# Kernel tuning notes

Measured on AMD Instinct MI355X. Metric: run time of the kernel, lower is better.

The kernel has to match this reference:

```python
import jax, jax.numpy as jnp
import numpy as np

G = 128          # number of point-cloud groups
DOWNSAMPLE = 256 # points per group
D = 256          # feature dim


def _pairwise_dist(x, y):
    # x: [G, n, d], y: [G, m, d] -> Euclidean distances [G, n, m]
    x2 = jnp.sum(x * x, axis=-1)[:, :, None]
    y2 = jnp.sum(y * y, axis=-1)[:, None, :]
    d2 = jnp.maximum(x2 + y2 - 2.0 * jnp.einsum('gnd,gmd->gnm', x, y), 0.0)
    # safe sqrt (zero diagonal has zero distance, avoid NaN grads)
    return jnp.where(d2 > 0, jnp.sqrt(jnp.where(d2 > 0, d2, 1.0)), 0.0)


def setup_inputs() -> dict:
    key = jax.random.key(0)
    k1, k2 = jax.random.split(key)
    inp = jax.random.normal(k1, (G * DOWNSAMPLE, D), dtype=jnp.float32)
    tgt = jax.random.normal(k2, (G * DOWNSAMPLE, D), dtype=jnp.float32)
    return {"input": inp, "target": tgt, "downsample": DOWNSAMPLE}


def reference(input, target, downsample):
    # MMDLoss.forward: reshape to (-1, downsample, D), batched energy distance, mean
    x = input.reshape(-1, downsample, input.shape[-1])   # [G, n, D]
    y = target.reshape(-1, downsample, target.shape[-1]) # [G, m, D]
    # Energy distance (geomloss 'energy' kernel k(x,y) = -||x-y||, uniform weights):
    # L = mean_ij ||x_i - y_j|| - 0.5 mean_ij ||x_i - x_j|| - 0.5 mean_ij ||y_i - y_j||
    d_xy = jnp.mean(_pairwise_dist(x, y), axis=(1, 2))  # [G]
    d_xx = jnp.mean(_pairwise_dist(x, x), axis=(1, 2))  # [G]
    d_yy = jnp.mean(_pairwise_dist(y, y), axis=(1, 2))  # [G]
    loss_per_group = d_xy - 0.5 * d_xx - 0.5 * d_yy
    return jnp.mean(loss_per_group)
```

## Files before the change

kernel.cpp:

```cpp
#include <hip/hip_runtime.h>
#include <hip/hip_bf16.h>
#include <stdint.h>
#include <string.h>

typedef __attribute__((ext_vector_type(8))) short short8;
typedef __attribute__((ext_vector_type(4))) float floatx4;

#define NPTS 256
#define DIM  256
#define TILE 128
#define BK   32
#define NIT  (DIM / BK)

static __device__ __forceinline__ uint32_t cvt2(float a, float b) {
    __hip_bfloat162 h = __float22bfloat162_rn(float2{a, b});
    uint32_t d;
    memcpy(&d, &h, 4);
    return d;
}
static __device__ __forceinline__ float sq8(const float4 u, const float4 v) {
    return u.x * u.x + u.y * u.y + u.z * u.z + u.w * u.w +
           v.x * v.x + v.y * v.y + v.z * v.z + v.w * v.w;
}

__global__ __launch_bounds__(512, 4)
void mmd_pipe(const float* __restrict__ X, const float* __restrict__ Y,
              float* __restrict__ out, float scale, int G) {
    int g, t;
    const int f = blockIdx.x;
    if ((G & 7) == 0) { const int xcd = f & 7, j = f >> 3; g = (j / 10) * 8 + xcd; t = j % 10; }
    else              { g = f / 10; t = f % 10; }

    int ptype, ti, tj; float w;
    if (t < 4)      { ptype = 0; ti = t >> 1; tj = t & 1; w = 1.0f; }
    else if (t < 7) { int u = t - 4; ptype = 1; ti = (u == 2); tj = (u >= 1); w = (u == 1) ? -1.0f : -0.5f; }
    else            { int u = t - 7; ptype = 2; ti = (u == 2); tj = (u >= 1); w = (u == 1) ? -1.0f : -0.5f; }

    const float *Pf, *Qf;
    if (ptype == 0)      { Pf = X; Qf = Y; }
    else if (ptype == 1) { Pf = X; Qf = X; }
    else                 { Pf = Y; Qf = Y; }
    const bool symdiag = (ptype != 0) && (ti == tj);

    const size_t prow0 = (size_t)g * NPTS + (size_t)ti * TILE;
    const size_t qrow0 = (size_t)g * NPTS + (size_t)tj * TILE;

    __shared__ __align__(16) uint16_t As[2][TILE * BK];
    __shared__ __align__(16) uint16_t Bs[2][TILE * BK];
    __shared__ float rnorm[TILE];
    __shared__ float cnorm[TILE];
    __shared__ float wpart[8];

    const int tid  = threadIdx.x;
    const int lane = tid & 63;
    const int wv   = tid >> 6;
    const int quad = lane >> 4;
    const int l15  = lane & 15;
    const int rowbase = (wv & 3) * 32;
    const int colbase = (wv >> 2) * 64;
    const int rsw = (quad ^ ((l15 >> 1) & 3)) * 8;

    const int prow = tid >> 2;
    const int pchk = tid & 3;
    const float* gA = Pf + (prow0 + prow) * DIM + pchk * 8;
    const int woff = prow * BK + ((pchk ^ ((prow >> 1) & 3)) * 8);

    floatx4 acc[2][4];
    #pragma unroll
    for (int i = 0; i < 2; ++i)
        #pragma unroll
        for (int j = 0; j < 4; ++j) acc[i][j] = (floatx4)0.0f;

    float sqp = 0.0f;

    if (symdiag) {
        float4 ra0 = *(const float4*)(gA);
        float4 ra1 = *(const float4*)(gA + 4);
        {
            uint4 pa;
            sqp += sq8(ra0, ra1);
            pa.x = cvt2(ra0.x, ra0.y); pa.y = cvt2(ra0.z, ra0.w);
            pa.z = cvt2(ra1.x, ra1.y); pa.w = cvt2(ra1.z, ra1.w);
            *(uint4*)&As[0][woff] = pa;
        }
        ra0 = *(const float4*)(gA + BK);
        ra1 = *(const float4*)(gA + BK + 4);

        #pragma unroll
        for (int it = 0; it < NIT; ++it) {
            const int b = it & 1;
            __syncthreads();

            short8 af[2], bfr[4];
            #pragma unroll
            for (int mi = 0; mi < 2; ++mi)
                af[mi] = *(const short8*)&As[b][(rowbase + mi * 16 + l15) * BK + rsw];
            #pragma unroll
            for (int ni = 0; ni < 4; ++ni)
                bfr[ni] = *(const short8*)&As[b][(colbase + ni * 16 + l15) * BK + rsw];

            if (it < NIT - 1) {
                uint4 pa;
                sqp += sq8(ra0, ra1);
                pa.x = cvt2(ra0.x, ra0.y); pa.y = cvt2(ra0.z, ra0.w);
                pa.z = cvt2(ra1.x, ra1.y); pa.w = cvt2(ra1.z, ra1.w);
                *(uint4*)&As[b ^ 1][woff] = pa;
            }
            if (it < NIT - 2) {
                const int k0 = (it + 2) * BK;
                ra0 = *(const float4*)(gA + k0);
                ra1 = *(const float4*)(gA + k0 + 4);
            }

            #pragma unroll
            for (int mi = 0; mi < 2; ++mi)
                #pragma unroll
                for (int ni = 0; ni < 4; ++ni)
                    acc[mi][ni] = __builtin_amdgcn_mfma_f32_16x16x32_bf16(
                        af[mi], bfr[ni], acc[mi][ni], 0, 0, 0);
        }

        sqp += __shfl_xor(sqp, 1); sqp += __shfl_xor(sqp, 2);
        if ((tid & 3) == 0) rnorm[prow] = sqp;
        __syncthreads();

        float lsum = 0.0f;
        #pragma unroll
        for (int mi = 0; mi < 2; ++mi) {
            #pragma unroll
            for (int i = 0; i < 4; ++i) {
                const int r = rowbase + mi * 16 + quad * 4 + i;
                const float rv = rnorm[r];
                #pragma unroll
                for (int ni = 0; ni < 4; ++ni) {
                    const int c = colbase + ni * 16 + l15;
                    float d2 = rv + rnorm[c] - 2.0f * acc[mi][ni][i];
                    float s = sqrtf(fmaxf(d2, 0.0f));
                    if (r == c) s = 0.0f;
                    lsum += s;
                }
            }
        }
        #pragma unroll
        for (int off = 32; off; off >>= 1) lsum += __shfl_down(lsum, off);
        if (lane == 0) wpart[wv] = lsum;
        __syncthreads();
        if (tid == 0) {
            float bs = 0.0f;
            #pragma unroll
            for (int i = 0; i < 8; ++i) bs += wpart[i];
            atomicAdd(out, bs * (w * scale));
        }
        return;
    }

    const float* gB = Qf + (qrow0 + prow) * DIM + pchk * 8;
    float sqq = 0.0f;

    float4 ra0 = *(const float4*)(gA);
    float4 ra1 = *(const float4*)(gA + 4);
    float4 rb0 = *(const float4*)(gB);
    float4 rb1 = *(const float4*)(gB + 4);
    {
        uint4 pa, pb;
        sqp += sq8(ra0, ra1);
        sqq += sq8(rb0, rb1);
        pa.x = cvt2(ra0.x, ra0.y); pa.y = cvt2(ra0.z, ra0.w);
        pa.z = cvt2(ra1.x, ra1.y); pa.w = cvt2(ra1.z, ra1.w);
        pb.x = cvt2(rb0.x, rb0.y); pb.y = cvt2(rb0.z, rb0.w);
        pb.z = cvt2(rb1.x, rb1.y); pb.w = cvt2(rb1.z, rb1.w);
        *(uint4*)&As[0][woff] = pa;
        *(uint4*)&Bs[0][woff] = pb;
    }
    ra0 = *(const float4*)(gA + BK);
    ra1 = *(const float4*)(gA + BK + 4);
    rb0 = *(const float4*)(gB + BK);
    rb1 = *(const float4*)(gB + BK + 4);

    #pragma unroll
    for (int it = 0; it < NIT; ++it) {
        const int b = it & 1;
        __syncthreads();

        short8 af[2], bfr[4];
        #pragma unroll
        for (int mi = 0; mi < 2; ++mi)
            af[mi] = *(const short8*)&As[b][(rowbase + mi * 16 + l15) * BK + rsw];
        #pragma unroll
        for (int ni = 0; ni < 4; ++ni)
            bfr[ni] = *(const short8*)&Bs[b][(colbase + ni * 16 + l15) * BK + rsw];

        if (it < NIT - 1) {
            uint4 pa, pb;
            sqp += sq8(ra0, ra1);
            sqq += sq8(rb0, rb1);
            pa.x = cvt2(ra0.x, ra0.y); pa.y = cvt2(ra0.z, ra0.w);
            pa.z = cvt2(ra1.x, ra1.y); pa.w = cvt2(ra1.z, ra1.w);
            pb.x = cvt2(rb0.x, rb0.y); pb.y = cvt2(rb0.z, rb0.w);
            pb.z = cvt2(rb1.x, rb1.y); pb.w = cvt2(rb1.z, rb1.w);
            *(uint4*)&As[b ^ 1][woff] = pa;
            *(uint4*)&Bs[b ^ 1][woff] = pb;
        }
        if (it < NIT - 2) {
            const int k0 = (it + 2) * BK;
            ra0 = *(const float4*)(gA + k0);
            ra1 = *(const float4*)(gA + k0 + 4);
            rb0 = *(const float4*)(gB + k0);
            rb1 = *(const float4*)(gB + k0 + 4);
        }

        #pragma unroll
        for (int mi = 0; mi < 2; ++mi)
            #pragma unroll
            for (int ni = 0; ni < 4; ++ni)
                acc[mi][ni] = __builtin_amdgcn_mfma_f32_16x16x32_bf16(
                    af[mi], bfr[ni], acc[mi][ni], 0, 0, 0);
    }

    sqp += __shfl_xor(sqp, 1); sqp += __shfl_xor(sqp, 2);
    sqq += __shfl_xor(sqq, 1); sqq += __shfl_xor(sqq, 2);
    if ((tid & 3) == 0) { rnorm[prow] = sqp; cnorm[prow] = sqq; }
    __syncthreads();

    float lsum = 0.0f;
    #pragma unroll
    for (int mi = 0; mi < 2; ++mi) {
        #pragma unroll
        for (int i = 0; i < 4; ++i) {
            const int r = rowbase + mi * 16 + quad * 4 + i;
            const float rv = rnorm[r];
            #pragma unroll
            for (int ni = 0; ni < 4; ++ni) {
                const int c = colbase + ni * 16 + l15;
                float d2 = rv + cnorm[c] - 2.0f * acc[mi][ni][i];
                float s = sqrtf(fmaxf(d2, 0.0f));
                lsum += s;
            }
        }
    }
    #pragma unroll
    for (int off = 32; off; off >>= 1) lsum += __shfl_down(lsum, off);
    if (lane == 0) wpart[wv] = lsum;
    __syncthreads();
    if (tid == 0) {
        float bs = 0.0f;
        #pragma unroll
        for (int i = 0; i < 8; ++i) bs += wpart[i];
        atomicAdd(out, bs * (w * scale));
    }
}

extern "C" void kernel_launch(void* const* d_in, const int* in_sizes, int n_in,
                              void* d_out, int out_size, void* d_ws, size_t ws_size,
                              hipStream_t stream) {
    const float* X = (const float*)d_in[0];
    const float* Y = (const float*)d_in[1];
    const int total_elems = in_sizes[0];
    const int G = total_elems / (NPTS * DIM);

    float* out = (float*)d_out;
    hipMemsetAsync(out, 0, sizeof(float) * out_size, stream);

    const float scale = 1.0f / ((float)NPTS * (float)NPTS * (float)G);
    mmd_pipe<<<10 * G, 512, 0, stream>>>(X, Y, out, scale, G);
}
```

Measured before the change: 115.6 us.

## Split into bf16 prep pass plus direct-to-LDS MFMA distance kernel

Adds a prep kernel that converts X and Y to bf16 once and computes row squared norms from the rounded values, storing both in global scratch. The main kernel then streams bf16 tiles straight into LDS using global_load_lds with a swizzled layout, double-buffered, and reuses the precomputed norms. This removes the repeated fp32 loads and per-tile conversions across the 10 tiles per group and halves the bytes the main kernel reads. The cost is an extra launch and an extra round trip through scratch memory.

Result: slower. 129.6 us (+12.1%).

```diff
diff --git a/kernel.cpp b/kernel.cpp
--- a/kernel.cpp
+++ b/kernel.cpp
@@ -5,13 +5,27 @@
 
 typedef __attribute__((ext_vector_type(8))) short short8;
 typedef __attribute__((ext_vector_type(4))) float floatx4;
+typedef unsigned short u16;
 
 #define NPTS 256
 #define DIM  256
 #define TILE 128
 #define BK   32
 #define NIT  (DIM / BK)
-
+#define GMAX 128
+
+__device__ __align__(16) static u16  g_Zb[(size_t)2 * GMAX * NPTS * DIM];
+__device__ static float              g_nrm[2 * GMAX * NPTS];
+
+static __device__ __forceinline__ uint32_t cvtsq2(float a, float b, float& s) {
+    __hip_bfloat162 h = __float22bfloat162_rn(float2{a, b});
+    uint32_t d;
+    memcpy(&d, &h, 4);
+    const float lo = __builtin_bit_cast(float, d << 16);
+    const float hi = __builtin_bit_cast(float, d & 0xFFFF0000u);
+    s += lo * lo + hi * hi;
+    return d;
+}
 static __device__ __forceinline__ uint32_t cvt2(float a, float b) {
     __hip_bfloat162 h = __float22bfloat162_rn(float2{a, b});
     uint32_t d;
@@ -21,6 +35,143 @@
 static __device__ __forceinline__ float sq8(const float4 u, const float4 v) {
     return u.x * u.x + u.y * u.y + u.z * u.z + u.w * u.w +
            v.x * v.x + v.y * v.y + v.z * v.z + v.w * v.w;
+}
+
+__global__ __launch_bounds__(256)
+void mmd_prep(const float* __restrict__ X, const float* __restrict__ Y,
+              int totalRows, int halfRows) {
+    const int gid = blockIdx.x * 256 + threadIdx.x;
+    const int row = gid >> 5;
+    if (row >= totalRows) return;
+    const int sub = gid & 31;
+    const float* src = (row < halfRows ? X + (size_t)row * DIM
+                                       : Y + (size_t)(row - halfRows) * DIM) + sub * 8;
+    const float4 a = *(const float4*)src;
+    const float4 b = *(const float4*)(src + 4);
+    float s = 0.0f;
+    uint4 p;
+    p.x = cvtsq2(a.x, a.y, s); p.y = cvtsq2(a.z, a.w, s);
+    p.z = cvtsq2(b.x, b.y, s); p.w = cvtsq2(b.z, b.w, s);
+    *(uint4*)(g_Zb + (size_t)row * DIM + sub * 8) = p;
+    s += __shfl_xor(s, 1); s += __shfl_xor(s, 2); s += __shfl_xor(s, 4);
+    s += __shfl_xor(s, 8); s += __shfl_xor(s, 16);
+    if (sub == 0) g_nrm[row] = s;
+}
+
+static __device__ __forceinline__ void stage_slice(
+    const u16* __restrict__ Zrow0, u16* ldsbase, int k0, int tid, int wv) {
+    const int srow = tid >> 2;
+    const int scs  = tid & 3;
+    const int scg  = scs ^ ((srow >> 1) & 3);
+    const u16* src = Zrow0 + (size_t)srow * DIM + k0 + scg * 8;
+    u16* dst = ldsbase + wv * 512;
+    __builtin_amdgcn_global_load_lds(
+        (const __attribute__((address_space(1))) uint32_t*)src,
+        (__attribute__((address_space(3))) uint32_t*)dst, 16, 0, 0);
+}
+
+__global__ __launch_bounds__(512, 4)
+void mmd_main(float* __restrict__ out, float scale, int G) {
+    int g, t;
+    const int f = blockIdx.x;
+    { const int xcd = f & 7, j = f >> 3; g = (j / 10) * 8 + xcd; t = j % 10; }
+
+    int ptype, ti, tj; float w;
+    if (t < 4)      { ptype = 0; ti = t >> 1; tj = t & 1; w = 1.0f; }
+    else if (t < 7) { int u = t - 4; ptype = 1; ti = (u == 2); tj = (u >= 1); w = (u == 1) ? -1.0f : -0.5f; }
+    else            { int u = t - 7; ptype = 2; ti = (u == 2); tj = (u >= 1); w = (u == 1) ? -1.0f : -0.5f; }
+
+    const int half = G * NPTS;
+    const int pbase = (ptype == 2) ? half : 0;
+    const int qbase = (ptype == 1) ? 0 : half;
+    const size_t prow0 = (size_t)pbase + (size_t)g * NPTS + (size_t)ti * TILE;
+    const size_t qrow0 = (size_t)qbase + (size_t)g * NPTS + (size_t)tj * TILE;
+    const bool symdiag = (ptype != 0) && (ti == tj);
+
+    const u16* ZP = g_Zb + prow0 * DIM;
+    const u16* ZQ = g_Zb + qrow0 * DIM;
+
+    __shared__ __align__(16) u16 As[2][TILE * BK];
+    __shared__ __align__(16) u16 Bs[2][TILE * BK];
+    __shared__ float rnormS[TILE];
+    __shared__ float cnormS[TILE];
+    __shared__ float wpart[8];
+
+    const int tid  = threadIdx.x;
+    const int lane = tid & 63;
+    const int wv   = tid >> 6;
+    const int quad = lane >> 4;
+    const int l15  = lane & 15;
+    const int rowbase = (wv & 3) * 32;
+    const int colbase = (wv >> 2) * 64;
+    const int rsw = (quad ^ ((l15 >> 1) & 3)) * 8;
+
+    floatx4 acc[2][4];
+    #pragma unroll
+    for (int i = 0; i < 2; ++i)
+        #pragma unroll
+        for (int j = 0; j < 4; ++j) acc[i][j] = (floatx4)0.0f;
+
+    if (tid < TILE)            rnormS[tid] = g_nrm[prow0 + tid];
+    else if (tid < 2 * TILE)   cnormS[tid - TILE] = g_nrm[qrow0 + (tid - TILE)];
+
+    stage_slice(ZP, As[0], 0, tid, wv);
+    if (!symdiag) stage_slice(ZQ, Bs[0], 0, tid, wv);
+
+    #pragma unroll
+    for (int it = 0; it < NIT; ++it) {
+        const int b = it & 1;
+        __syncthreads();
+
+        if (it + 1 < NIT) {
+            stage_slice(ZP, As[b ^ 1], (it + 1) * BK, tid, wv);
+            if (!symdiag) stage_slice(ZQ, Bs[b ^ 1], (it + 1) * BK, tid, wv);
+        }
+
+        const u16* ab = As[b];
+        const u16* bb = symdiag ? As[b] : Bs[b];
+        short8 af[2], bfr[4];
+        #pragma unroll
+        for (int mi = 0; mi < 2; ++mi)
+            af[mi] = *(const short8*)&ab[(rowbase + mi * 16 + l15) * BK + rsw];
+        #pragma unroll
+        for (int ni = 0; ni < 4; ++ni)
+            bfr[ni] = *(const short8*)&bb[(colbase + ni * 16 + l15) * BK + rsw];
+        #pragma unroll
+        for (int mi = 0; mi < 2; ++mi)
+            #pragma unroll
+            for (int ni = 0; ni < 4; ++ni)
+                acc[mi][ni] = __builtin_amdgcn_mfma_f32_16x16x32_bf16(
+                    af[mi], bfr[ni], acc[mi][ni], 0, 0, 0);
+    }
+
+    float lsum = 0.0f;
+    #pragma unroll
+    for (int mi = 0; mi < 2; ++mi) {
+        #pragma unroll
+        for (int i = 0; i < 4; ++i) {
+            const int r = rowbase + mi * 16 + quad * 4 + i;
+            const float rv = rnormS[r];
+            #pragma unroll
+            for (int ni = 0; ni < 4; ++ni) {
+                const int c = colbase + ni * 16 + l15;
+                float d2 = rv + cnormS[c] - 2.0f * acc[mi][ni][i];
+                float s = sqrtf(fmaxf(d2, 0.0f));
+                if (symdiag && (r == c)) s = 0.0f;
+                lsum += s;
+            }
+        }
+    }
+    #pragma unroll
+    for (int off = 32; off; off >>= 1) lsum += __shfl_down(lsum, off);
+    if (lane == 0) wpart[wv] = lsum;
+    __syncthreads();
+    if (tid == 0) {
+        float bs = 0.0f;
+        #pragma unroll
+        for (int i = 0; i < 8; ++i) bs += wpart[i];
+        atomicAdd(out, bs * (w * scale));
+    }
 }
 
 __global__ __launch_bounds__(512, 4)
@@ -262,5 +413,12 @@
     hipMemsetAsync(out, 0, sizeof(float) * out_size, stream);
 
     const float scale = 1.0f / ((float)NPTS * (float)NPTS * (float)G);
-    mmd_pipe<<<10 * G, 512, 0, stream>>>(X, Y, out, scale, G);
-}
+
+    if (G <= GMAX && (G & 7) == 0) {
+        const int rows = 2 * G * NPTS;
+        mmd_prep<<<rows / 8, 256, 0, stream>>>(X, Y, rows, G * NPTS);
+        mmd_main<<<10 * G, 512, 0, stream>>>(out, scale, G);
+    } else {
+        mmd_pipe<<<10 * G, 512, 0, stream>>>(X, Y, out, scale, G);
+    }
+}
```
